# Kernel optimization log

Measured on AMD Instinct MI355X. Metric: run time of the kernel, lower is better.

Reference implementation:

```python
import jax, jax.numpy as jnp
import numpy as np

EMB_W, COMMIT_W, ENT_W = 1.0, 0.25, 0.1  # loss weights from init_kwargs


def setup_inputs() -> dict:
    key = jax.random.key(0)
    k1, k2 = jax.random.split(key)
    B, H, W, D, K = 32, 32, 32, 64, 1024
    inputs = jax.random.normal(k1, (B, H, W, D), dtype=jnp.float32)
    # keras RandomUniform default: U(-0.05, 0.05)
    codebook = jax.random.uniform(k2, (K, D), dtype=jnp.float32, minval=-0.05, maxval=0.05)
    return {"inputs": inputs, "codebook": codebook}


def reference(inputs, codebook):
    # inputs: [B,H,W,D], codebook: [K,D]
    D = inputs.shape[-1]
    x = inputs.reshape(-1, D)  # [N,D]
    dist = (
        jnp.sum(x * x, axis=-1, keepdims=True)
        - 2.0 * (x @ codebook.T)
        + jnp.sum(codebook * codebook, axis=-1)
    )  # [N,K]
    tokens = jnp.argmin(dist, axis=-1)  # [N]
    emb = codebook[tokens].reshape(inputs.shape)  # [B,H,W,D]

    embedding_loss = EMB_W * jnp.mean((jax.lax.stop_gradient(emb) - inputs) ** 2)
    commitment_loss = COMMIT_W * jnp.mean((emb - jax.lax.stop_gradient(inputs)) ** 2)
    # 'entropy' loss as written in call(): mean over codebook of per-code min distance
    entropy_loss = ENT_W * jnp.mean(jnp.min(dist, axis=0))
    loss = embedding_loss + commitment_loss + entropy_loss

    # training=True path: straight-through estimator
    out = inputs + jax.lax.stop_gradient(emb - inputs)
    return out, loss
```

## Files before the change

kernel.cpp:

```cpp
#include <hip/hip_runtime.h>
#include <math.h>

#define NROWS 32768
#define NCODE 1024
#define AMB_CAP 8192
#define GAP_THRESH 1.5e-4f

typedef __attribute__((ext_vector_type(8))) short bf16x8;
typedef __attribute__((ext_vector_type(4))) float f32x4;

__device__ __forceinline__ unsigned short bf16_rne(float f) {
    unsigned u = __float_as_uint(f);
    unsigned r = u + 0x7FFFu + ((u >> 16) & 1u);
    return (unsigned short)(r >> 16);
}

typedef const __attribute__((address_space(1))) unsigned GU;
typedef __attribute__((address_space(3))) unsigned LU;
__device__ __forceinline__ void gl_lds16(const void* g, void* l) {
    __builtin_amdgcn_global_load_lds((GU*)g, (LU*)l, 16, 0, 0);
}
__device__ __forceinline__ void gl_lds4(const void* g, void* l) {
    __builtin_amdgcn_global_load_lds((GU*)g, (LU*)l, 4, 0, 0);
}

__global__ __launch_bounds__(64) void vq_prep(
    const float* __restrict__ cb, float* __restrict__ cn4,
    unsigned* __restrict__ minK, unsigned* __restrict__ counter,
    float* __restrict__ gsumsq, unsigned* __restrict__ ticket,
    unsigned short* __restrict__ wsB)
{
    int c = blockIdx.x * 64 + threadIdx.x;
    if (c == 0) { *counter = 0u; *gsumsq = 0.f; *ticket = 0u; }
    float v[64];
    const float4* src = (const float4*)(cb + (size_t)c * 64);
    float s = 0.f;
    #pragma unroll
    for (int i = 0; i < 16; i++) {
        float4 t = src[i];
        v[i*4+0] = t.x; v[i*4+1] = t.y; v[i*4+2] = t.z; v[i*4+3] = t.w;
        s += t.x*t.x + t.y*t.y + t.z*t.z + t.w*t.w;
    }
    cn4[c] = s + 4.0f;
    minK[c] = 0x7F800000u;
    int cc = c >> 6, ct = (c >> 4) & 3, cl = c & 15;
    #pragma unroll
    for (int q = 0; q < 4; q++) {
        int half = q & 1, lo = q >> 1;
        #pragma unroll
        for (int g = 0; g < 4; g++) {
            unsigned short u8[8] __attribute__((aligned(16)));
            #pragma unroll
            for (int j = 0; j < 8; j++) {
                float f = v[half*32 + g*8 + j];
                unsigned short h = bf16_rne(f);
                if (lo) h = bf16_rne(f - __uint_as_float((unsigned)h << 16));
                u8[j] = h;
            }
            size_t off = (size_t)cc * 8192 + ct * 2048 + q * 512 + (g * 16 + cl) * 8;
            *(uint4*)(wsB + off) = *(const uint4*)u8;
        }
    }
}

__global__ __launch_bounds__(512, 4) void vq_main(
    const float* __restrict__ x, const float* __restrict__ cb,
    const unsigned short* __restrict__ wsB, const float* __restrict__ cn4,
    float* __restrict__ out, unsigned* __restrict__ minK,
    unsigned* __restrict__ counter, int* __restrict__ amb,
    float* __restrict__ gsumsq)
{
    __shared__ __align__(16) unsigned char Bb[2][32768];
    __shared__ float cn4L[2][128];
    __shared__ unsigned scrE[1024];
    __shared__ float mD1[128], mD2[128];
    __shared__ int   mI1[128];
    __shared__ int   tokS[64];
    __shared__ float redS[8];

    const int tid = threadIdx.x;
    const int lane = tid & 63;
    const int wi = tid >> 6;
    const int g = wi >> 1;
    const int h = wi & 1;
    const int ln15 = lane & 15;
    const int q = lane >> 4;
    const int row0 = blockIdx.x * 64;
    const int rot = blockIdx.x & 7;

    scrE[tid] = 0x7F800000u;
    scrE[512 + tid] = 0x7F800000u;

    const char* wsBb = (const char*)wsB;
    {
        int wbase = (tid & ~63) * 16;
        #pragma unroll
        for (int i = 0; i < 4; i++)
            gl_lds16(wsBb + (size_t)rot*32768 + (i*512 + tid)*16,
                     (void*)&Bb[0][i*8192 + wbase]);
        if (wi == 0) {
            gl_lds4(cn4 + rot*128 + lane,      (void*)&cn4L[0][0]);
            gl_lds4(cn4 + rot*128 + 64 + lane, (void*)&cn4L[0][64]);
        }
    }

    bf16x8 Ah0, Ah1, Al0, Al1;
    float xnm4[4];
    {
        const float* xr = x + (size_t)(row0 + g*16 + ln15) * 64 + q * 8;
        float4 f0 = *(const float4*)xr;
        float4 f1 = *(const float4*)(xr + 4);
        float4 f2 = *(const float4*)(xr + 32);
        float4 f3 = *(const float4*)(xr + 36);
        float fa[8] = {f0.x,f0.y,f0.z,f0.w,f1.x,f1.y,f1.z,f1.w};
        float fb[8] = {f2.x,f2.y,f2.z,f2.w,f3.x,f3.y,f3.z,f3.w};
        unsigned short hh8[8] __attribute__((aligned(16)));
        unsigned short ll8[8] __attribute__((aligned(16)));
        unsigned short h28[8] __attribute__((aligned(16)));
        unsigned short l28[8] __attribute__((aligned(16)));
        float ss = 0.f;
        #pragma unroll
        for (int j = 0; j < 8; j++) {
            ss += fa[j]*fa[j] + fb[j]*fb[j];
            unsigned short hh = bf16_rne(fa[j]);
            hh8[j] = hh; ll8[j] = bf16_rne(fa[j] - __uint_as_float((unsigned)hh << 16));
            hh = bf16_rne(fb[j]);
            h28[j] = hh; l28[j] = bf16_rne(fb[j] - __uint_as_float((unsigned)hh << 16));
        }
        Ah0 = *(const bf16x8*)hh8; Al0 = *(const bf16x8*)ll8;
        Ah1 = *(const bf16x8*)h28; Al1 = *(const bf16x8*)l28;
        ss += __shfl_xor(ss, 16);
        ss += __shfl_xor(ss, 32);
        #pragma unroll
        for (int r = 0; r < 4; r++)
            xnm4[r] = __shfl(ss, (q << 2) | r, 64) - 4.0f;
    }

    float d1[4], d2[4];
    int   i1[4];
    #pragma unroll
    for (int r = 0; r < 4; r++) { d1[r] = INFINITY; d2[r] = INFINITY; i1[r] = 0; }

    for (int s = 0; s < 8; s++) {
        __syncthreads();
        const int cb_ = s & 1, nb = (s + 1) & 1;
        const int cphys = (s + rot) & 7;
        if (s < 7) {
            const int cnx = (s + 1 + rot) & 7;
            int wbase = (tid & ~63) * 16;
            #pragma unroll
            for (int i = 0; i < 4; i++)
                gl_lds16(wsBb + (size_t)cnx*32768 + (i*512 + tid)*16,
                         (void*)&Bb[nb][i*8192 + wbase]);
            if (wi == 0) {
                gl_lds4(cn4 + cnx*128 + lane,      (void*)&cn4L[nb][0]);
                gl_lds4(cn4 + cnx*128 + 64 + lane, (void*)&cn4L[nb][64]);
            }
        }
        const unsigned char* buf = Bb[cb_];
        #pragma unroll
        for (int lct = 0; lct < 4; lct++) {
            const int ct = 4*h + lct;
            const unsigned char* tb = buf + (ct >> 2)*16384 + (ct & 3)*4096;
            bf16x8 Bh0 = *(const bf16x8*)(tb +    0 + lane*16);
            bf16x8 Bh1 = *(const bf16x8*)(tb + 1024 + lane*16);
            bf16x8 Bl0 = *(const bf16x8*)(tb + 2048 + lane*16);
            bf16x8 Bl1 = *(const bf16x8*)(tb + 3072 + lane*16);
            float cn4v = cn4L[cb_][ct*16 + ln15];
            int kid = cphys*128 + ct*16 + ln15;
            f32x4 z = {0.f, 0.f, 0.f, 0.f};
            f32x4 acc0 = __builtin_amdgcn_mfma_f32_16x16x32_bf16(Ah0, Bh0, z, 0, 0, 0);
            f32x4 acc1 = __builtin_amdgcn_mfma_f32_16x16x32_bf16(Ah1, Bh1, z, 0, 0, 0);
            acc0 = __builtin_amdgcn_mfma_f32_16x16x32_bf16(Ah0, Bl0, acc0, 0, 0, 0);
            acc1 = __builtin_amdgcn_mfma_f32_16x16x32_bf16(Ah1, Bl1, acc1, 0, 0, 0);
            acc0 = __builtin_amdgcn_mfma_f32_16x16x32_bf16(Al0, Bh0, acc0, 0, 0, 0);
            acc1 = __builtin_amdgcn_mfma_f32_16x16x32_bf16(Al1, Bh1, acc1, 0, 0, 0);
            float cminv = INFINITY;
            #pragma unroll
            for (int r = 0; r < 4; r++) {
                float sdot = acc0[r] + acc1[r];
                float wv = fmaf(sdot, -2.0f, cn4v);
                bool lt = wv < d1[r];
                d2[r] = lt ? d1[r] : fminf(d2[r], wv);
                i1[r] = lt ? kid   : i1[r];
                d1[r] = lt ? wv    : d1[r];
                cminv = fminf(cminv, wv + xnm4[r]);
            }
            cminv = fminf(cminv, __shfl_xor(cminv, 16));
            cminv = fminf(cminv, __shfl_xor(cminv, 32));
            if (q == lct) atomicMin(&scrE[kid], __float_as_uint(cminv));
        }
    }
    __syncthreads();

    #pragma unroll
    for (int d = 1; d < 16; d <<= 1) {
        #pragma unroll
        for (int r = 0; r < 4; r++) {
            float od1 = __shfl_xor(d1[r], d);
            int   oi1 = __shfl_xor(i1[r], d);
            float od2 = __shfl_xor(d2[r], d);
            bool take = (od1 < d1[r]) || (od1 == d1[r] && oi1 < i1[r]);
            float loser = take ? d1[r] : od1;
            d2[r] = fminf(fminf(d2[r], od2), loser);
            d1[r] = take ? od1 : d1[r];
            i1[r] = take ? oi1 : i1[r];
        }
    }
    if (ln15 == 0) {
        #pragma unroll
        for (int r = 0; r < 4; r++) {
            int idx = (g*16 + q*4 + r) * 2 + h;
            mD1[idx] = d1[r]; mI1[idx] = i1[r]; mD2[idx] = d2[r];
        }
    }
    __syncthreads();

    if (tid < 64) {
        float a1 = mD1[tid*2],   b1 = mD1[tid*2+1];
        int   ai = mI1[tid*2],   bi = mI1[tid*2+1];
        float a2 = mD2[tid*2],   b2 = mD2[tid*2+1];
        bool ta = (a1 < b1) || (a1 == b1 && ai < bi);
        float D1 = ta ? a1 : b1;
        int   I1 = ta ? ai : bi;
        float D2 = ta ? fminf(a2, b1) : fminf(b2, a1);
        tokS[tid] = I1;
        if (D2 - D1 < GAP_THRESH) {
            unsigned idx = atomicAdd(counter, 1u);
            if (idx < AMB_CAP) { amb[2*idx] = row0 + tid; amb[2*idx+1] = I1; }
        }
    }

    {
        unsigned u0 = scrE[tid];
        if (u0 < minK[tid]) atomicMin(&minK[tid], u0);
        unsigned u1 = scrE[512 + tid];
        if (u1 < minK[512 + tid]) atomicMin(&minK[512 + tid], u1);
    }
    __syncthreads();

    {
        float acc2 = 0.f;
        #pragma unroll
        for (int uu = 0; uu < 2; uu++) {
            int u = uu*512 + tid;
            int row = u >> 4, c4 = u & 15;
            int tok = tokS[row];
            float4 c = ((const float4*)(cb + (size_t)tok*64))[c4];
            float4 xx = ((const float4*)(x + (size_t)(row0 + row)*64))[c4];
            ((float4*)(out + (size_t)(row0 + row)*64))[c4] = c;
            float dx = c.x-xx.x, dy = c.y-xx.y, dz = c.z-xx.z, dw = c.w-xx.w;
            acc2 += dx*dx + dy*dy + dz*dz + dw*dw;
        }
        #pragma unroll
        for (int o = 32; o > 0; o >>= 1) acc2 += __shfl_down(acc2, o);
        if (lane == 0) redS[wi] = acc2;
        __syncthreads();
        if (tid == 0) {
            float t = 0.f;
            #pragma unroll
            for (int w = 0; w < 8; w++) t += redS[w];
            atomicAdd(gsumsq, t);
        }
    }
}

__global__ __launch_bounds__(256) void vq_tail(
    const float* __restrict__ x, const float* __restrict__ cb,
    float* __restrict__ out, const unsigned* __restrict__ counter,
    const int* __restrict__ amb, float* __restrict__ gsumsq,
    unsigned* __restrict__ ticket, const unsigned* __restrict__ minK,
    float* __restrict__ out_loss)
{
    __shared__ __align__(16) float cbS[16384];
    __shared__ double xs[64];
    __shared__ double bd[256];
    __shared__ int    bi[256];
    __shared__ unsigned lastS;
    __shared__ float redS[4];

    const int tid = threadIdx.x;

    unsigned cnt = *counter; if (cnt > AMB_CAP) cnt = AMB_CAP;
    for (unsigned i = blockIdx.x; i < cnt; i += gridDim.x) {
        int row = amb[2*i], oldk = amb[2*i+1];
        __syncthreads();
        if (tid < 64) xs[tid] = (double)x[(size_t)row*64 + tid];
        __syncthreads();
        double xn = 0.0;
        #pragma unroll 8
        for (int d = 0; d < 64; d++) xn += xs[d]*xs[d];
        double best = INFINITY; int bk = 1 << 30;
        for (int b = 0; b < 4; b++) {
            __syncthreads();
            #pragma unroll
            for (int k = 0; k < 16; k++)
                ((float4*)cbS)[k*256 + tid] = ((const float4*)cb)[b*4096 + k*256 + tid];
            __syncthreads();
            int kcode = b*256 + tid;
            const int t6 = tid & 63;
            double dot = 0.0, cn2 = 0.0;
            #pragma unroll 8
            for (int dd = 0; dd < 64; dd++) {
                int d = (dd + t6) & 63;
                double cv = (double)cbS[tid*64 + d];
                dot = fma(xs[d], cv, dot);
                cn2 = fma(cv, cv, cn2);
            }
            double dist = (xn - 2.0*dot) + cn2;
            if (dist < best || (dist == best && kcode < bk)) { best = dist; bk = kcode; }
        }
        bd[tid] = best; bi[tid] = bk;
        __syncthreads();
        for (int s = 128; s > 0; s >>= 1) {
            if (tid < s) {
                double od = bd[tid+s]; int ok = bi[tid+s];
                if (od < bd[tid] || (od == bd[tid] && ok < bi[tid])) { bd[tid] = od; bi[tid] = ok; }
            }
            __syncthreads();
        }
        int bestk = bi[0];
        if (bestk != oldk) {
            double part = 0.0;
            if (tid < 64) {
                float cn = cb[(size_t)bestk*64 + tid];
                float co = cb[(size_t)oldk*64 + tid];
                out[(size_t)row*64 + tid] = cn;
                double dn = (double)cn - xs[tid];
                double dl = (double)co - xs[tid];
                part = dn*dn - dl*dl;
            }
            __syncthreads();
            bd[tid] = part;
            __syncthreads();
            for (int s = 128; s > 0; s >>= 1) {
                if (tid < s) bd[tid] += bd[tid+s];
                __syncthreads();
            }
            if (tid == 0) atomicAdd(gsumsq, (float)bd[0]);
        }
    }

    __syncthreads();
    if (tid == 0) {
        __threadfence();
        lastS = (atomicAdd(ticket, 1u) == 63u) ? 1u : 0u;
    }
    __syncthreads();
    if (lastS) {
        __threadfence();
        float s = 0.f;
        #pragma unroll
        for (int jj = 0; jj < 4; jj++)
            s += __uint_as_float(minK[jj*256 + tid]);
        #pragma unroll
        for (int o = 32; o > 0; o >>= 1) s += __shfl_down(s, o);
        if ((tid & 63) == 0) redS[tid >> 6] = s;
        __syncthreads();
        if (tid == 0) {
            float gs = atomicAdd(gsumsq, 0.0f);
            float tot = redS[0] + redS[1] + redS[2] + redS[3];
            out_loss[0] = 1.25f * (gs / 2097152.0f) + 0.1f * (tot / 1024.0f);
        }
    }
}

extern "C" void kernel_launch(void* const* d_in, const int* in_sizes, int n_in,
                              void* d_out, int out_size, void* d_ws, size_t ws_size,
                              hipStream_t stream) {
    const float* x  = (const float*)d_in[0];
    const float* cb = (const float*)d_in[1];
    float* out = (float*)d_out;

    char* ws = (char*)d_ws;
    unsigned*       counter = (unsigned*)ws;
    float*          gsumsq  = (float*)(ws + 4);
    unsigned*       ticket  = (unsigned*)(ws + 8);
    float*          cn4     = (float*)(ws + 1024);
    unsigned*       minK    = (unsigned*)(ws + 8192);
    int*            amb     = (int*)(ws + 16384);
    unsigned short* wsB     = (unsigned short*)(ws + 131072);

    vq_prep<<<16,  64,  0, stream>>>(cb, cn4, minK, counter, gsumsq, ticket, wsB);
    vq_main<<<512, 512, 0, stream>>>(x, cb, wsB, cn4, out, minK, counter, amb, gsumsq);
    vq_tail<<<64,  256, 0, stream>>>(x, cb, out, counter, amb, gsumsq, ticket, minK,
                                     out + 2097152);
}
```

Before: 114.7 us.

## Split codebook across two blocks per row tile and merge partial argmins in tail

The main kernel now launches twice as many blocks, each scanning half the codebook (512 codes) for a 64-row tile. This halves LDS use per block and raises parallelism and occupancy. Per-half best/second-best distances and indices are written to workspace, and the tail kernel merges the halves, gathers codebook rows, and computes squared error. Ambiguous rows are rechecked locally per tail block (capped at 32) rather than through a global atomic list. The global float atomics are replaced by per-block partial sums reduced by the last block, at the cost of extra global traffic for the half results.

```diff
diff --git a/kernel.cpp b/kernel.cpp
--- a/kernel.cpp
+++ b/kernel.cpp
@@ -3,7 +3,6 @@
 
 #define NROWS 32768
 #define NCODE 1024
-#define AMB_CAP 8192
 #define GAP_THRESH 1.5e-4f
 
 typedef __attribute__((ext_vector_type(8))) short bf16x8;
@@ -26,12 +25,11 @@
 
 __global__ __launch_bounds__(64) void vq_prep(
     const float* __restrict__ cb, float* __restrict__ cn4,
-    unsigned* __restrict__ minK, unsigned* __restrict__ counter,
-    float* __restrict__ gsumsq, unsigned* __restrict__ ticket,
+    unsigned* __restrict__ minK, unsigned* __restrict__ ticket,
     unsigned short* __restrict__ wsB)
 {
     int c = blockIdx.x * 64 + threadIdx.x;
-    if (c == 0) { *counter = 0u; *gsumsq = 0.f; *ticket = 0u; }
+    if (c == 0) *ticket = 0u;
     float v[64];
     const float4* src = (const float4*)(cb + (size_t)c * 64);
     float s = 0.f;
@@ -64,19 +62,15 @@
 }
 
 __global__ __launch_bounds__(512, 4) void vq_main(
-    const float* __restrict__ x, const float* __restrict__ cb,
-    const unsigned short* __restrict__ wsB, const float* __restrict__ cn4,
-    float* __restrict__ out, unsigned* __restrict__ minK,
-    unsigned* __restrict__ counter, int* __restrict__ amb,
-    float* __restrict__ gsumsq)
+    const float* __restrict__ x, const unsigned short* __restrict__ wsB,
+    const float* __restrict__ cn4, unsigned* __restrict__ minK,
+    float* __restrict__ hD1, int* __restrict__ hI1, float* __restrict__ hD2)
 {
-    __shared__ __align__(16) unsigned char Bb[2][32768];
-    __shared__ float cn4L[2][128];
-    __shared__ unsigned scrE[1024];
+    __shared__ __align__(16) unsigned char Bb[2][16384];
+    __shared__ float cn4L[2][64];
+    __shared__ unsigned scrE[512];
     __shared__ float mD1[128], mD2[128];
     __shared__ int   mI1[128];
-    __shared__ int   tokS[64];
-    __shared__ float redS[8];
 
     const int tid = threadIdx.x;
     const int lane = tid & 63;
@@ -85,23 +79,21 @@
     const int h = wi & 1;
     const int ln15 = lane & 15;
     const int q = lane >> 4;
-    const int row0 = blockIdx.x * 64;
-    const int rot = blockIdx.x & 7;
+    const int b = blockIdx.x;
+    const int ch = b & 1;
+    const int row0 = (b >> 1) * 64;
+    const int rot = (b >> 1) & 7;
 
     scrE[tid] = 0x7F800000u;
-    scrE[512 + tid] = 0x7F800000u;
 
     const char* wsBb = (const char*)wsB;
     {
         int wbase = (tid & ~63) * 16;
         #pragma unroll
-        for (int i = 0; i < 4; i++)
-            gl_lds16(wsBb + (size_t)rot*32768 + (i*512 + tid)*16,
+        for (int i = 0; i < 2; i++)
+            gl_lds16(wsBb + (size_t)(ch*8 + rot)*16384 + (i*512 + tid)*16,
                      (void*)&Bb[0][i*8192 + wbase]);
-        if (wi == 0) {
-            gl_lds4(cn4 + rot*128 + lane,      (void*)&cn4L[0][0]);
-            gl_lds4(cn4 + rot*128 + 64 + lane, (void*)&cn4L[0][64]);
-        }
+        if (wi == 0) gl_lds4(cn4 + (ch*8 + rot)*64 + lane, (void*)&cn4L[0][0]);
     }
 
     bf16x8 Ah0, Ah1, Al0, Al1;
@@ -149,25 +141,23 @@
             const int cnx = (s + 1 + rot) & 7;
             int wbase = (tid & ~63) * 16;
             #pragma unroll
-            for (int i = 0; i < 4; i++)
-                gl_lds16(wsBb + (size_t)cnx*32768 + (i*512 + tid)*16,
+            for (int i = 0; i < 2; i++)
+                gl_lds16(wsBb + (size_t)(ch*8 + cnx)*16384 + (i*512 + tid)*16,
                          (void*)&Bb[nb][i*8192 + wbase]);
-            if (wi == 0) {
-                gl_lds4(cn4 + cnx*128 + lane,      (void*)&cn4L[nb][0]);
-                gl_lds4(cn4 + cnx*128 + 64 + lane, (void*)&cn4L[nb][64]);
-            }
+            if (wi == 0) gl_lds4(cn4 + (ch*8 + cnx)*64 + lane, (void*)&cn4L[nb][0]);
         }
         const unsigned char* buf = Bb[cb_];
         #pragma unroll
-        for (int lct = 0; lct < 4; lct++) {
-            const int ct = 4*h + lct;
-            const unsigned char* tb = buf + (ct >> 2)*16384 + (ct & 3)*4096;
+        for (int lct = 0; lct < 2; lct++) {
+            const int ct = 2*h + lct;
+            const unsigned char* tb = buf + ct*4096;
             bf16x8 Bh0 = *(const bf16x8*)(tb +    0 + lane*16);
             bf16x8 Bh1 = *(const bf16x8*)(tb + 1024 + lane*16);
             bf16x8 Bl0 = *(const bf16x8*)(tb + 2048 + lane*16);
             bf16x8 Bl1 = *(const bf16x8*)(tb + 3072 + lane*16);
             float cn4v = cn4L[cb_][ct*16 + ln15];
-            int kid = cphys*128 + ct*16 + ln15;
+            int kloc = cphys*64 + ct*16 + ln15;
+            int kid  = ch*512 + kloc;
             f32x4 z = {0.f, 0.f, 0.f, 0.f};
             f32x4 acc0 = __builtin_amdgcn_mfma_f32_16x16x32_bf16(Ah0, Bh0, z, 0, 0, 0);
             f32x4 acc1 = __builtin_amdgcn_mfma_f32_16x16x32_bf16(Ah1, Bh1, z, 0, 0, 0);
@@ -188,7 +178,7 @@
             }
             cminv = fminf(cminv, __shfl_xor(cminv, 16));
             cminv = fminf(cminv, __shfl_xor(cminv, 32));
-            if (q == lct) atomicMin(&scrE[kid], __float_as_uint(cminv));
+            if (q == lct) atomicMin(&scrE[kloc], __float_as_uint(cminv));
         }
     }
     __syncthreads();
@@ -221,69 +211,86 @@
         int   ai = mI1[tid*2],   bi = mI1[tid*2+1];
         float a2 = mD2[tid*2],   b2 = mD2[tid*2+1];
         bool ta = (a1 < b1) || (a1 == b1 && ai < bi);
+        size_t o = (size_t)ch*NROWS + row0 + tid;
+        hD1[o] = ta ? a1 : b1;
+        hI1[o] = ta ? ai : bi;
+        hD2[o] = ta ? fminf(a2, b1) : fminf(b2, a1);
+    }
+
+    {
+        unsigned u0 = scrE[tid];
+        if (u0 < minK[ch*512 + tid]) atomicMin(&minK[ch*512 + tid], u0);
+    }
+}
+
+__global__ __launch_bounds__(256) void vq_tail(
+    const float* __restrict__ x, const float* __restrict__ cb,
+    float* __restrict__ out, const float* __restrict__ hD1,
+    const int* __restrict__ hI1, const float* __restrict__ hD2,
+    const unsigned* __restrict__ minK, float* __restrict__ sumsqP,
+    float* __restrict__ deltaP, unsigned* __restrict__ ticket,
+    float* __restrict__ out_loss)
+{
+    __shared__ __align__(16) float cbS[16384];
+    __shared__ double xs[64];
+    __shared__ double bd[256];
+    __shared__ int    bix[256];
+    __shared__ int    tokS[128];
+    __shared__ int    listRow[32], listTok[32];
+    __shared__ int    lcnt;
+    __shared__ double deltaS;
+    __shared__ unsigned lastS;
+    __shared__ float redS[4], redS2[4];
+
+    const int tid = threadIdx.x;
+    const int lane = tid & 63;
+    const int w = tid >> 6;
+    const int b = blockIdx.x;
+    const int rb0 = b * 128;
+
+    if (tid == 0) { lcnt = 0; deltaS = 0.0; }
+    __syncthreads();
+
+    if (tid < 128) {
+        int row = rb0 + tid;
+        float a1 = hD1[row],         b1 = hD1[NROWS + row];
+        int   ai = hI1[row],         bi = hI1[NROWS + row];
+        float a2 = hD2[row],         b2 = hD2[NROWS + row];
+        bool ta = (a1 < b1) || (a1 == b1 && ai < bi);
         float D1 = ta ? a1 : b1;
         int   I1 = ta ? ai : bi;
         float D2 = ta ? fminf(a2, b1) : fminf(b2, a1);
         tokS[tid] = I1;
         if (D2 - D1 < GAP_THRESH) {
-            unsigned idx = atomicAdd(counter, 1u);
-            if (idx < AMB_CAP) { amb[2*idx] = row0 + tid; amb[2*idx+1] = I1; }
-        }
-    }
-
-    {
-        unsigned u0 = scrE[tid];
-        if (u0 < minK[tid]) atomicMin(&minK[tid], u0);
-        unsigned u1 = scrE[512 + tid];
-        if (u1 < minK[512 + tid]) atomicMin(&minK[512 + tid], u1);
+            int idx = atomicAdd(&lcnt, 1);
+            if (idx < 32) { listRow[idx] = row; listTok[idx] = I1; }
+        }
     }
     __syncthreads();
 
     {
         float acc2 = 0.f;
         #pragma unroll
-        for (int uu = 0; uu < 2; uu++) {
-            int u = uu*512 + tid;
+        for (int j = 0; j < 8; j++) {
+            int u = j*256 + tid;
             int row = u >> 4, c4 = u & 15;
             int tok = tokS[row];
             float4 c = ((const float4*)(cb + (size_t)tok*64))[c4];
-            float4 xx = ((const float4*)(x + (size_t)(row0 + row)*64))[c4];
-            ((float4*)(out + (size_t)(row0 + row)*64))[c4] = c;
+            float4 xx = ((const float4*)(x + (size_t)(rb0 + row)*64))[c4];
+            ((float4*)(out + (size_t)(rb0 + row)*64))[c4] = c;
             float dx = c.x-xx.x, dy = c.y-xx.y, dz = c.z-xx.z, dw = c.w-xx.w;
             acc2 += dx*dx + dy*dy + dz*dz + dw*dw;
         }
         #pragma unroll
         for (int o = 32; o > 0; o >>= 1) acc2 += __shfl_down(acc2, o);
-        if (lane == 0) redS[wi] = acc2;
-        __syncthreads();
-        if (tid == 0) {
-            float t = 0.f;
-            #pragma unroll
-            for (int w = 0; w < 8; w++) t += redS[w];
-            atomicAdd(gsumsq, t);
-        }
-    }
-}
-
-__global__ __launch_bounds__(256) void vq_tail(
-    const float* __restrict__ x, const float* __restrict__ cb,
-    float* __restrict__ out, const unsigned* __restrict__ counter,
-    const int* __restrict__ amb, float* __restrict__ gsumsq,
-    unsigned* __restrict__ ticket, const unsigned* __restrict__ minK,
-    float* __restrict__ out_loss)
-{
-    __shared__ __align__(16) float cbS[16384];
-    __shared__ double xs[64];
-    __shared__ double bd[256];
-    __shared__ int    bi[256];
-    __shared__ unsigned lastS;
-    __shared__ float redS[4];
-
-    const int tid = threadIdx.x;
-
-    unsigned cnt = *counter; if (cnt > AMB_CAP) cnt = AMB_CAP;
-    for (unsigned i = blockIdx.x; i < cnt; i += gridDim.x) {
-        int row = amb[2*i], oldk = amb[2*i+1];
+        if (lane == 0) redS[w] = acc2;
+        __syncthreads();
+        if (tid == 0) sumsqP[b] = redS[0] + redS[1] + redS[2] + redS[3];
+    }
+
+    int nfix = lcnt < 32 ? lcnt : 32;
+    for (int i = 0; i < nfix; i++) {
+        int row = listRow[i], oldk = listTok[i];
         __syncthreads();
         if (tid < 64) xs[tid] = (double)x[(size_t)row*64 + tid];
         __syncthreads();
@@ -291,13 +298,13 @@
         #pragma unroll 8
         for (int d = 0; d < 64; d++) xn += xs[d]*xs[d];
         double best = INFINITY; int bk = 1 << 30;
-        for (int b = 0; b < 4; b++) {
+        for (int bb = 0; bb < 4; bb++) {
             __syncthreads();
             #pragma unroll
             for (int k = 0; k < 16; k++)
-                ((float4*)cbS)[k*256 + tid] = ((const float4*)cb)[b*4096 + k*256 + tid];
+                ((float4*)cbS)[k*256 + tid] = ((const float4*)cb)[bb*4096 + k*256 + tid];
             __syncthreads();
-            int kcode = b*256 + tid;
+            int kcode = bb*256 + tid;
             const int t6 = tid & 63;
             double dot = 0.0, cn2 = 0.0;
             #pragma unroll 8
@@ -310,16 +317,16 @@
             double dist = (xn - 2.0*dot) + cn2;
             if (dist < best || (dist == best && kcode < bk)) { best = dist; bk = kcode; }
         }
-        bd[tid] = best; bi[tid] = bk;
+        bd[tid] = best; bix[tid] = bk;
         __syncthreads();
         for (int s = 128; s > 0; s >>= 1) {
             if (tid < s) {
-                double od = bd[tid+s]; int ok = bi[tid+s];
-                if (od < bd[tid] || (od == bd[tid] && ok < bi[tid])) { bd[tid] = od; bi[tid] = ok; }
+                double od = bd[tid+s]; int ok = bix[tid+s];
+                if (od < bd[tid] || (od == bd[tid] && ok < bix[tid])) { bd[tid] = od; bix[tid] = ok; }
             }
             __syncthreads();
         }
-        int bestk = bi[0];
+        int bestk = bix[0];
         if (bestk != oldk) {
             double part = 0.0;
             if (tid < 64) {
@@ -337,30 +344,35 @@
                 if (tid < s) bd[tid] += bd[tid+s];
                 __syncthreads();
             }
-            if (tid == 0) atomicAdd(gsumsq, (float)bd[0]);
-        }
-    }
+            if (tid == 0) deltaS += bd[0];
+        }
+    }
+    __syncthreads();
+    if (tid == 0) deltaP[b] = (float)deltaS;
 
     __syncthreads();
     if (tid == 0) {
         __threadfence();
-        lastS = (atomicAdd(ticket, 1u) == 63u) ? 1u : 0u;
+        lastS = (atomicAdd(ticket, 1u) == 255u) ? 1u : 0u;
     }
     __syncthreads();
     if (lastS) {
         __threadfence();
-        float s = 0.f;
+        volatile const float* sp = sumsqP;
+        volatile const float* dp = deltaP;
+        float sq = sp[tid] + dp[tid];
+        float es = 0.f;
         #pragma unroll
         for (int jj = 0; jj < 4; jj++)
-            s += __uint_as_float(minK[jj*256 + tid]);
-        #pragma unroll
-        for (int o = 32; o > 0; o >>= 1) s += __shfl_down(s, o);
-        if ((tid & 63) == 0) redS[tid >> 6] = s;
+            es += __uint_as_float(minK[jj*256 + tid]);
+        #pragma unroll
+        for (int o = 32; o > 0; o >>= 1) { sq += __shfl_down(sq, o); es += __shfl_down(es, o); }
+        if (lane == 0) { redS[w] = sq; redS2[w] = es; }
         __syncthreads();
         if (tid == 0) {
-            float gs = atomicAdd(gsumsq, 0.0f);
-            float tot = redS[0] + redS[1] + redS[2] + redS[3];
-            out_loss[0] = 1.25f * (gs / 2097152.0f) + 0.1f * (tot / 1024.0f);
+            float S = redS[0] + redS[1] + redS[2] + redS[3];
+            float E = redS2[0] + redS2[1] + redS2[2] + redS2[3];
+            out_loss[0] = 1.25f * (S / 2097152.0f) + 0.1f * (E / 1024.0f);
         }
     }
 }
@@ -373,16 +385,18 @@
     float* out = (float*)d_out;
 
     char* ws = (char*)d_ws;
-    unsigned*       counter = (unsigned*)ws;
-    float*          gsumsq  = (float*)(ws + 4);
-    unsigned*       ticket  = (unsigned*)(ws + 8);
-    float*          cn4     = (float*)(ws + 1024);
-    unsigned*       minK    = (unsigned*)(ws + 8192);
-    int*            amb     = (int*)(ws + 16384);
-    unsigned short* wsB     = (unsigned short*)(ws + 131072);
-
-    vq_prep<<<16,  64,  0, stream>>>(cb, cn4, minK, counter, gsumsq, ticket, wsB);
-    vq_main<<<512, 512, 0, stream>>>(x, cb, wsB, cn4, out, minK, counter, amb, gsumsq);
-    vq_tail<<<64,  256, 0, stream>>>(x, cb, out, counter, amb, gsumsq, ticket, minK,
-                                     out + 2097152);
-}
+    unsigned*       ticket = (unsigned*)ws;
+    unsigned*       minK   = (unsigned*)(ws + 1024);
+    float*          sumsqP = (float*)(ws + 8192);
+    float*          deltaP = (float*)(ws + 12288);
+    float*          cn4    = (float*)(ws + 16384);
+    float*          hD1    = (float*)(ws + 32768);
+    int*            hI1    = (int*)(ws + 294912);
+    float*          hD2    = (float*)(ws + 557056);
+    unsigned short* wsB    = (unsigned short*)(ws + 819200);
+
+    vq_prep<<<16,   64,  0, stream>>>(cb, cn4, minK, ticket, wsB);
+    vq_main<<<1024, 512, 0, stream>>>(x, wsB, cn4, minK, hD1, hI1, hD2);
+    vq_tail<<<256,  256, 0, stream>>>(x, cb, out, hD1, hI1, hD2, minK, sumsqP,
+                                      deltaP, ticket, out + 2097152);
+}
```

Measured after the change: 135.0 us. 1.18x slower.
